# Kernel tuning notes

Hardware: AMD Instinct MI355X
Metric: run time of the kernel (lower is better)

Reference implementation:

```python
import jax, jax.numpy as jnp
import numpy as np

B, T, C, HS = 512, 256, 384, 64  # batch, block_size, n_embed, head_size


def setup_inputs() -> dict:
    key = jax.random.key(0)
    kx, kq, kk, kv = jax.random.split(key, 4)
    x = jax.random.normal(kx, (B, T, C), dtype=jnp.float32)
    # Linear(n_embed, head_size, bias=False) weights stored as [in, out]
    s = 1.0 / np.sqrt(C)
    Wq = jax.random.normal(kq, (C, HS), dtype=jnp.float32) * s
    Wk = jax.random.normal(kk, (C, HS), dtype=jnp.float32) * s
    Wv = jax.random.normal(kv, (C, HS), dtype=jnp.float32) * s
    return {"x": x, "Wq": Wq, "Wk": Wk, "Wv": Wv}


def reference(x, Wq, Wk, Wv):
    Bb, Tt, Cc = x.shape
    q = jnp.einsum('btc,ch->bth', x, Wq)
    k = jnp.einsum('btc,ch->bth', x, Wk)
    v = jnp.einsum('btc,ch->bth', x, Wv)
    # NOTE: original scales by C**-0.5 (embed dim), NOT head_size**-0.5
    wei = jnp.einsum('bqh,bkh->bqk', q, k) * (Cc ** -0.5)
    # causal mask: tril == 0 (strict upper triangle) -> -inf
    causal = jnp.tril(jnp.ones((Tt, Tt), dtype=bool))
    wei = jnp.where(causal[None, :, :], wei, -jnp.inf)
    # NOTE: original applies softmax over dim=1 (query axis) — replicated faithfully
    wei = jax.nn.softmax(wei, axis=1)
    out = jnp.einsum('bqk,bkh->bqh', wei, v)
    return out
```

## Files before the change

### kernel.cpp

```cpp
#include <hip/hip_runtime.h>

typedef float  f32x4  __attribute__((ext_vector_type(4)));
typedef __bf16 bf16x8 __attribute__((ext_vector_type(8)));

#define CC 384

__device__ __forceinline__ unsigned short f2bf(float f) {
  union { float f; unsigned int u; } x; x.f = f;
  unsigned int u = x.u;
  return (unsigned short)((u + 0x7fffu + ((u >> 16) & 1u)) >> 16);
}

__device__ __forceinline__ f32x4 mfma16(bf16x8 a, bf16x8 b, f32x4 c) {
  return __builtin_amdgcn_mfma_f32_16x16x32_bf16(a, b, c, 0, 0, 0);
}

__global__ void repack_w(const float* __restrict__ Wq, const float* __restrict__ Wk,
                         const float* __restrict__ Wv, unsigned short* __restrict__ wf) {
  int e = blockIdx.x * 512 + threadIdx.x;
  int k = e / 192;
  int n = e - k * 192;
  const float* W = (n < 64) ? Wq : (n < 128) ? Wk : Wv;
  float val = W[k * 64 + (n & 63)];
  int kk = k >> 5;
  int lane = (((k >> 3) & 3) << 4) | (n & 15);
  int j = k & 7;
  int nt = n >> 4;
  wf[(size_t)(((kk * 12 + nt) << 6) + lane) * 8 + j] = f2bf(val);
}

__global__ __launch_bounds__(512, 2) void fused(const float* __restrict__ x,
                                                const unsigned short* __restrict__ wf,
                                                float* __restrict__ out) {
  __shared__ __attribute__((aligned(16))) unsigned char smem[119808];
  unsigned short (*Sx)[72] = (unsigned short(*)[72])smem;
  unsigned short (*kL)[72] = (unsigned short(*)[72])(smem + 36864);
  unsigned short (*vT)[264] = (unsigned short(*)[264])(smem + 73728);
  float* pm = (float*)(smem + 107520);
  float* ps = pm + 1024;
  float* gg = ps + 1024;

  const int tid = threadIdx.x;
  const int w = tid >> 6, lane = tid & 63;
  const int l15 = lane & 15, lhi = lane >> 4;
  const int b = blockIdx.x;
  const int mts[2] = {w, 15 - w};

  const float* xr0 = x + ((size_t)b * 256 + mts[0] * 16 + l15) * CC + lhi * 8;
  const float* xr1 = x + ((size_t)b * 256 + mts[1] * 16 + l15) * CC + lhi * 8;
  const unsigned short* wl = wf + lane * 8;

  f32x4 zero = {0.f, 0.f, 0.f, 0.f};
  f32x4 acc[2][12];
#pragma unroll
  for (int i = 0; i < 2; ++i)
#pragma unroll
    for (int nt = 0; nt < 12; ++nt) acc[i][nt] = zero;

  {
    bf16x8 wreg[2][12];
    f32x4  xreg[2][4];

#define LOADW(kp_, s_) do {                                                     \
    _Pragma("unroll")                                                           \
    for (int nt_ = 0; nt_ < 12; ++nt_)                                          \
      wreg[s_][nt_] = *(const bf16x8*)(wl + ((kp_) * 12 + nt_) * 512);          \
  } while (0)
#define LOADX(kp_, s_) do {                                                     \
    const int o_ = (kp_) * 32;                                                  \
    xreg[s_][0] = *(const f32x4*)(xr0 + o_);                                    \
    xreg[s_][1] = *(const f32x4*)(xr0 + o_ + 4);                                \
    xreg[s_][2] = *(const f32x4*)(xr1 + o_);                                    \
    xreg[s_][3] = *(const f32x4*)(xr1 + o_ + 4);                                \
  } while (0)

    LOADW(0, 0);
    LOADX(0, 0);
#pragma unroll
    for (int kp = 0; kp < 12; ++kp) {
      const int cur = kp & 1, nxt = cur ^ 1;
      if (kp < 11) { LOADW(kp + 1, nxt); LOADX(kp + 1, nxt); }
#pragma unroll
      for (int i = 0; i < 2; ++i) {
        bf16x8 af;
#pragma unroll
        for (int j = 0; j < 4; ++j) {
          af[j]     = (__bf16)xreg[cur][2 * i][j];
          af[4 + j] = (__bf16)xreg[cur][2 * i + 1][j];
        }
#pragma unroll
        for (int nt = 0; nt < 12; ++nt) acc[i][nt] = mfma16(af, wreg[cur][nt], acc[i][nt]);
      }
    }
#undef LOADW
#undef LOADX
  }

  const float qs = 0.05103103630798288f;
#pragma unroll
  for (int i = 0; i < 2; ++i) {
    const int rb = mts[i] * 16 + lhi * 4;
#pragma unroll
    for (int nt = 0; nt < 4; ++nt) {
      const int h = nt * 16 + l15;
#pragma unroll
      for (int r = 0; r < 4; ++r) Sx[rb + r][h] = f2bf(acc[i][nt][r] * qs);
    }
#pragma unroll
    for (int nt = 4; nt < 8; ++nt) {
      const int h = (nt - 4) * 16 + l15;
#pragma unroll
      for (int r = 0; r < 4; ++r) kL[rb + r][h] = f2bf(acc[i][nt][r]);
    }
#pragma unroll
    for (int nt = 8; nt < 12; ++nt) {
      const int h = (nt - 8) * 16 + l15;
      unsigned long long pk =
          (unsigned long long)f2bf(acc[i][nt][0]) |
          ((unsigned long long)f2bf(acc[i][nt][1]) << 16) |
          ((unsigned long long)f2bf(acc[i][nt][2]) << 32) |
          ((unsigned long long)f2bf(acc[i][nt][3]) << 48);
      *(unsigned long long*)&vT[h][rb] = pk;
    }
  }
  __syncthreads();

  bf16x8 qf[2][2];
#pragma unroll
  for (int i = 0; i < 2; ++i)
#pragma unroll
    for (int kk = 0; kk < 2; ++kk)
      qf[i][kk] = *(const bf16x8*)&Sx[mts[i] * 16 + l15][kk * 32 + lhi * 8];

  f32x4 oacc[2][4];
#pragma unroll
  for (int i = 0; i < 2; ++i)
#pragma unroll
    for (int nh = 0; nh < 4; ++nh) oacc[i][nh] = zero;

  for (int p = 0; p < 4; ++p) {
    const int p4 = 4 * p;
    const bool any = (mts[1] >= p4);
    if (any) {
      bf16x8 kf[4][2];
#pragma unroll
      for (int c = 0; c < 4; ++c)
#pragma unroll
        for (int kk = 0; kk < 2; ++kk)
          kf[c][kk] = *(const bf16x8*)&kL[p * 64 + c * 16 + l15][kk * 32 + lhi * 8];
#pragma unroll
      for (int i = 0; i < 2; ++i) {
        const int mt = mts[i];
        if (mt < p4) continue;
        const int cmax = mt - p4;
        const int rowb = mt * 16 + lhi * 4;
#pragma unroll
        for (int c = 0; c < 4; ++c) {
          const int cs = c * 16 + l15;
          if (c <= cmax) {
            f32x4 s = zero;
            s = mfma16(qf[i][0], kf[c][0], s);
            s = mfma16(qf[i][1], kf[c][1], s);
            const int cg = p * 64 + cs;
            const bool v0 = (rowb + 0) >= cg, v1 = (rowb + 1) >= cg;
            const bool v2 = (rowb + 2) >= cg, v3 = (rowb + 3) >= cg;
            float m = -1e30f;
            m = fmaxf(m, v0 ? s[0] : -1e30f);
            m = fmaxf(m, v1 ? s[1] : -1e30f);
            m = fmaxf(m, v2 ? s[2] : -1e30f);
            m = fmaxf(m, v3 ? s[3] : -1e30f);
            m = fmaxf(m, __shfl_xor(m, 16));
            m = fmaxf(m, __shfl_xor(m, 32));
            const float e0 = v0 ? __expf(s[0] - m) : 0.f;
            const float e1 = v1 ? __expf(s[1] - m) : 0.f;
            const float e2 = v2 ? __expf(s[2] - m) : 0.f;
            const float e3 = v3 ? __expf(s[3] - m) : 0.f;
            float t = e0 + e1 + e2 + e3;
            t += __shfl_xor(t, 16);
            t += __shfl_xor(t, 32);
            Sx[rowb + 0][cs] = f2bf(e0);
            Sx[rowb + 1][cs] = f2bf(e1);
            Sx[rowb + 2][cs] = f2bf(e2);
            Sx[rowb + 3][cs] = f2bf(e3);
            if (lhi == 0) { pm[mt * 64 + cs] = m; ps[mt * 64 + cs] = t; }
          } else {
            if (lhi == 0) { pm[mt * 64 + cs] = -1e30f; ps[mt * 64 + cs] = 0.f; }
          }
        }
      }
    }
    __syncthreads();
    {
      float M = -1e30f;
      for (int mt = p4; mt < 16; ++mt) M = fmaxf(M, pm[mt * 64 + lane]);
      float L = 0.f;
      for (int mt = p4; mt < 16; ++mt) L += ps[mt * 64 + lane] * __expf(pm[mt * 64 + lane] - M);
      const float rv = 1.0f / L;
      int mtw = p4 + w;
      if (mtw < 16) gg[mtw * 64 + lane] = __expf(pm[mtw * 64 + lane] - M) * rv;
      mtw += 8;
      if (mtw < 16) gg[mtw * 64 + lane] = __expf(pm[mtw * 64 + lane] - M) * rv;
    }
    __syncthreads();
    if (any) {
      bf16x8 vf[4][2];
#pragma unroll
      for (int nh = 0; nh < 4; ++nh)
#pragma unroll
        for (int kk = 0; kk < 2; ++kk)
          vf[nh][kk] = *(const bf16x8*)&vT[nh * 16 + l15][p * 64 + kk * 32 + lhi * 8];
#pragma unroll
      for (int i = 0; i < 2; ++i) {
        const int mt = mts[i];
        if (mt < p4) continue;
        const int grow = mt * 16 + l15;
        const int dmax = mt - p4;
#pragma unroll
        for (int kk = 0; kk < 2; ++kk) {
          if (kk == 1 && dmax <= 1) continue;
          const int c0 = kk * 32 + lhi * 8;
          bf16x8 se = *(const bf16x8*)&Sx[grow][c0];
          f32x4 gA = *(const f32x4*)&gg[mt * 64 + c0];
          f32x4 gB = *(const f32x4*)&gg[mt * 64 + c0 + 4];
          const int cg0 = p * 64 + c0;
          bf16x8 wfr;
#pragma unroll
          for (int j = 0; j < 4; ++j)
            wfr[j] = (cg0 + j <= grow) ? (__bf16)((float)se[j] * gA[j]) : (__bf16)0.f;
#pragma unroll
          for (int j = 0; j < 4; ++j)
            wfr[4 + j] = (cg0 + 4 + j <= grow) ? (__bf16)((float)se[4 + j] * gB[j]) : (__bf16)0.f;
#pragma unroll
          for (int nh = 0; nh < 4; ++nh) oacc[i][nh] = mfma16(wfr, vf[nh][kk], oacc[i][nh]);
        }
      }
    }
  }
#pragma unroll
  for (int i = 0; i < 2; ++i) {
    const int rb = mts[i] * 16 + lhi * 4;
#pragma unroll
    for (int nh = 0; nh < 4; ++nh) {
      const int h = nh * 16 + l15;
#pragma unroll
      for (int r = 0; r < 4; ++r)
        out[(size_t)b * 16384 + (size_t)(rb + r) * 64 + h] = oacc[i][nh][r];
    }
  }
}

extern "C" void kernel_launch(void* const* d_in, const int* in_sizes, int n_in,
                              void* d_out, int out_size, void* d_ws, size_t ws_size,
                              hipStream_t stream) {
  const float* x  = (const float*)d_in[0];
  const float* Wq = (const float*)d_in[1];
  const float* Wk = (const float*)d_in[2];
  const float* Wv = (const float*)d_in[3];
  float* out = (float*)d_out;

  unsigned short* wf = (unsigned short*)d_ws;

  repack_w<<<144, 512, 0, stream>>>(Wq, Wk, Wv, wf);
  fused<<<512, 512, 0, stream>>>(x, wf, out);
}
```

Measured before the change: 90.57 us.

## Stage QKV weights into LDS via async global_load_lds triple buffering

Each wave used to load the packed bf16 weight fragments for every k-step directly from global memory into registers. Now the whole block cooperatively streams weight chunks into shared memory with global_load_lds, triple-buffered with manual vmcnt waits and barriers. The k-step is widened to 64 columns of x, halving the loop trip count. This removes redundant per-wave global weight traffic and frees the registers that held the weights, at the cost of block-wide barriers each iteration and fragile hand-tuned waitcnt accounting. The staging buffer reuses the Sx region, and a syncthreads is added before Sx is written.

```diff
diff --git a/kernel.cpp b/kernel.cpp
--- a/kernel.cpp
+++ b/kernel.cpp
@@ -4,6 +4,8 @@
 typedef __bf16 bf16x8 __attribute__((ext_vector_type(8)));
 
 #define CC 384
+#define AS1 __attribute__((address_space(1)))
+#define AS3 __attribute__((address_space(3)))
 
 __device__ __forceinline__ unsigned short f2bf(float f) {
   union { float f; unsigned int u; } x; x.f = f;
@@ -39,6 +41,7 @@
   float* pm = (float*)(smem + 107520);
   float* ps = pm + 1024;
   float* gg = ps + 1024;
+  unsigned short* wst = (unsigned short*)smem;
 
   const int tid = threadIdx.x;
   const int w = tid >> 6, lane = tid & 63;
@@ -48,7 +51,6 @@
 
   const float* xr0 = x + ((size_t)b * 256 + mts[0] * 16 + l15) * CC + lhi * 8;
   const float* xr1 = x + ((size_t)b * 256 + mts[1] * 16 + l15) * CC + lhi * 8;
-  const unsigned short* wl = wf + lane * 8;
 
   f32x4 zero = {0.f, 0.f, 0.f, 0.f};
   f32x4 acc[2][12];
@@ -57,44 +59,64 @@
 #pragma unroll
     for (int nt = 0; nt < 12; ++nt) acc[i][nt] = zero;
 
-  {
-    bf16x8 wreg[2][12];
-    f32x4  xreg[2][4];
-
-#define LOADW(kp_, s_) do {                                                     \
-    _Pragma("unroll")                                                           \
-    for (int nt_ = 0; nt_ < 12; ++nt_)                                          \
-      wreg[s_][nt_] = *(const bf16x8*)(wl + ((kp_) * 12 + nt_) * 512);          \
+  f32x4 xreg[2][8];
+
+#define WSTAGE(kp_, b_) do {                                                                  \
+    const unsigned short* s_ = wf + (size_t)(kp_) * 12288 + tid * 8;                          \
+    unsigned short* d_ = wst + (b_) * 12288 + tid * 8;                                        \
+    __builtin_amdgcn_global_load_lds((const AS1 void*)(s_),        (AS3 void*)(d_),        16, 0, 0); \
+    __builtin_amdgcn_global_load_lds((const AS1 void*)(s_ + 4096), (AS3 void*)(d_ + 4096), 16, 0, 0); \
+    __builtin_amdgcn_global_load_lds((const AS1 void*)(s_ + 8192), (AS3 void*)(d_ + 8192), 16, 0, 0); \
   } while (0)
-#define LOADX(kp_, s_) do {                                                     \
-    const int o_ = (kp_) * 32;                                                  \
-    xreg[s_][0] = *(const f32x4*)(xr0 + o_);                                    \
-    xreg[s_][1] = *(const f32x4*)(xr0 + o_ + 4);                                \
-    xreg[s_][2] = *(const f32x4*)(xr1 + o_);                                    \
-    xreg[s_][3] = *(const f32x4*)(xr1 + o_ + 4);                                \
+#define XLOAD(kp_, s_) do {                                                                   \
+    const int o_ = (kp_) * 64;                                                                \
+    xreg[s_][0] = *(const f32x4*)(xr0 + o_);      xreg[s_][1] = *(const f32x4*)(xr0 + o_ + 4);  \
+    xreg[s_][2] = *(const f32x4*)(xr0 + o_ + 32); xreg[s_][3] = *(const f32x4*)(xr0 + o_ + 36); \
+    xreg[s_][4] = *(const f32x4*)(xr1 + o_);      xreg[s_][5] = *(const f32x4*)(xr1 + o_ + 4);  \
+    xreg[s_][6] = *(const f32x4*)(xr1 + o_ + 32); xreg[s_][7] = *(const f32x4*)(xr1 + o_ + 36); \
   } while (0)
 
-    LOADW(0, 0);
-    LOADX(0, 0);
-#pragma unroll
-    for (int kp = 0; kp < 12; ++kp) {
-      const int cur = kp & 1, nxt = cur ^ 1;
-      if (kp < 11) { LOADW(kp + 1, nxt); LOADX(kp + 1, nxt); }
-#pragma unroll
-      for (int i = 0; i < 2; ++i) {
+  WSTAGE(0, 0);
+  WSTAGE(1, 1);
+  XLOAD(0, 0);
+  __builtin_amdgcn_sched_barrier(0);
+  asm volatile("s_waitcnt vmcnt(11)" ::: "memory");
+  __builtin_amdgcn_s_barrier();
+  __builtin_amdgcn_sched_barrier(0);
+
+#pragma unroll
+  for (int kp = 0; kp < 6; ++kp) {
+    const int cur = kp & 1, nxt = cur ^ 1;
+    if (kp < 5) XLOAD(kp + 1, nxt);
+    if (kp < 4) WSTAGE(kp + 2, (kp + 2) % 3);
+    __builtin_amdgcn_sched_barrier(0);
+    const unsigned short* base = wst + (kp % 3) * 12288;
+#pragma unroll
+    for (int i = 0; i < 2; ++i) {
+#pragma unroll
+      for (int k2 = 0; k2 < 2; ++k2) {
         bf16x8 af;
 #pragma unroll
         for (int j = 0; j < 4; ++j) {
-          af[j]     = (__bf16)xreg[cur][2 * i][j];
-          af[4 + j] = (__bf16)xreg[cur][2 * i + 1][j];
+          af[j]     = (__bf16)xreg[cur][i * 4 + k2 * 2][j];
+          af[4 + j] = (__bf16)xreg[cur][i * 4 + k2 * 2 + 1][j];
         }
-#pragma unroll
-        for (int nt = 0; nt < 12; ++nt) acc[i][nt] = mfma16(af, wreg[cur][nt], acc[i][nt]);
+        const bf16x8* bp = (const bf16x8*)(base + k2 * 6144) + lane;
+#pragma unroll
+        for (int nt = 0; nt < 12; ++nt) acc[i][nt] = mfma16(af, bp[nt * 64], acc[i][nt]);
       }
     }
-#undef LOADW
-#undef LOADX
-  }
+    __builtin_amdgcn_sched_barrier(0);
+    if (kp < 4)       asm volatile("s_waitcnt vmcnt(11)" ::: "memory");
+    else if (kp == 4) asm volatile("s_waitcnt vmcnt(8)" ::: "memory");
+    if (kp < 5) {
+      __builtin_amdgcn_s_barrier();
+      __builtin_amdgcn_sched_barrier(0);
+    }
+  }
+#undef WSTAGE
+#undef XLOAD
+  __syncthreads();
 
   const float qs = 0.05103103630798288f;
 #pragma unroll
```

New measurement: 91.63 us. Within noise of the previous version (+1.2%).
